# Kernel tuning notes

Hardware: AMD Instinct MI355X
Metric: run time of the kernel (lower is better)

## Reference

```python
import jax, jax.numpy as jnp
import numpy as np
import math
from jax import lax

D = 256      # d_model = out_channel
NH = 8       # n_heads
DEP = D // NH
DFF = 1024
B = 48       # conv batch == attended axis in this model
CIN = 32
HW = 32
S = 30 * 30  # (HW-2)**2 after 3x3 valid conv
OUT = 1
FMAX = float(np.finfo(np.float32).max)


def _p(k, shp, scale=0.02):
    return jax.random.normal(k, shp, jnp.float32) * scale


def setup_inputs():
    key = jax.random.key(0)
    ks = jax.random.split(key, 34)
    return {
        'X_en': jax.random.normal(ks[0], (B, CIN, HW, HW), jnp.float32),
        'X_de': jax.random.normal(ks[1], (B, CIN, HW, HW), jnp.float32),
        'conv1_w': _p(ks[2], (D, CIN, 3, 3)), 'conv1_b': _p(ks[3], (D,)),
        'conv2_w': _p(ks[4], (D, D, 3, 3)), 'conv2_b': _p(ks[5], (D,)),
        'enc_wq': _p(ks[6], (D, D)), 'enc_wk': _p(ks[7], (D, D)), 'enc_wv': _p(ks[8], (D, D)),
        'enc_rel_w': _p(ks[9], (S, NH, DEP, B)),
        'enc_ffn_w1': _p(ks[10], (DFF, D)), 'enc_ffn_b1': _p(ks[11], (DFF,)),
        'enc_ffn_w2': _p(ks[12], (D, DFF)), 'enc_ffn_b2': _p(ks[13], (D,)),
        'dec_m_wq': _p(ks[14], (D, D)), 'dec_m_wk': _p(ks[15], (D, D)), 'dec_m_wv': _p(ks[16], (D, D)),
        'dec_m_rel_w': _p(ks[17], (S, NH, DEP, B)),
        'dec_m_lin1_w': _p(ks[18], (B, B)), 'dec_m_lin1_b': _p(ks[19], (B,)),
        'dec_m_lin2_w': _p(ks[20], (B, B)), 'dec_m_lin2_b': _p(ks[21], (B,)),
        'dec_c_wq': _p(ks[22], (D, D)), 'dec_c_wk': _p(ks[23], (D, D)), 'dec_c_wv': _p(ks[24], (D, D)),
        'dec_c_rel_w': _p(ks[25], (S, NH, DEP, B)),
        'dec_ffn_w1': _p(ks[26], (DFF, D)), 'dec_ffn_b1': _p(ks[27], (DFF,)),
        'dec_ffn_w2': _p(ks[28], (D, DFF)), 'dec_ffn_b2': _p(ks[29], (D,)),
        'out_w': _p(ks[30], (OUT, D)), 'out_b': _p(ks[31], (OUT,)),
    }


def _ln(x, eps=1e-5):
    m = jnp.mean(x, -1, keepdims=True)
    v = jnp.mean((x - m) ** 2, -1, keepdims=True)
    return (x - m) / jnp.sqrt(v + eps)


def _skew(q, w):
    # Music-Transformer relative-position skew: matmul + pad + reshape + slice
    emd = jnp.einsum('shbd,shdj->shbj', q, w)  # (S,NH,b,b)
    s, h, i, j = emd.shape
    l = i + j - 1
    x = jnp.concatenate([emd, jnp.zeros_like(emd)], -1).reshape(s, h, -1)
    pad = (-x.shape[-1]) % l
    x = jnp.pad(x, ((0, 0), (0, 0), (0, pad)))
    return x.reshape(s, h, -1, l)[:, :, :i, i - 1:]


def _mha(xq, xk, xv, wq, wk, wv, rel_w, lins=None):
    b, sl, d = xq.shape
    # raw view (not transpose): (b,sl,d) -> (sl,b,NH,DEP), then swap to (sl,NH,b,DEP)
    q = (xq @ wq.T).reshape(sl, b, NH, DEP).swapaxes(1, 2)
    k = (xk @ wk.T).reshape(sl, b, NH, DEP).swapaxes(1, 2)
    v = (xv @ wv.T).reshape(sl, b, NH, DEP).swapaxes(1, 2)
    scores = jnp.einsum('shid,shjd->shij', q, k) / math.sqrt(DEP)  # (sl,NH,b,b)
    if lins is not None:  # masked path: per-call linears + causal mask
        l1w, l1b, l2w, l2b = lins
        qk = scores @ l1w.T + l1b
        qk = jnp.swapaxes(qk, 2, 3) @ l2w.T + l2b
        mask = jnp.triu(jnp.full((b, b), -FMAX, jnp.float32), 1)
        bmm = qk + mask
    else:
        bmm = scores  # linear1/linear2 outputs are discarded when mask=False
    attn = jax.nn.softmax(bmm + _skew(q, rel_w), axis=0)  # softmax over dim 0 (S)
    out = jnp.einsum('shij,shjd->shid', attn, v)  # (sl,NH,b,DEP)
    return out.reshape(b, sl, NH * DEP)  # view(a_s[2], a_s[0], -1)


def reference(X_en, X_de, conv1_w, conv1_b, conv2_w, conv2_b, enc_wq, enc_wk, enc_wv, enc_rel_w, enc_ffn_w1, enc_ffn_b1, enc_ffn_w2, enc_ffn_b2, dec_m_wq, dec_m_wk, dec_m_wv, dec_m_rel_w, dec_m_lin1_w, dec_m_lin1_b, dec_m_lin2_w, dec_m_lin2_b, dec_c_wq, dec_c_wk, dec_c_wv, dec_c_rel_w, dec_ffn_w1, dec_ffn_b1, dec_ffn_w2, dec_ffn_b2, out_w, out_b):
    def conv(x, w, b_, pad):
        y = lax.conv_general_dilated(x, w, (1, 1), [(pad, pad), (pad, pad)],
                                     dimension_numbers=('NCHW', 'OIHW', 'NCHW'))
        return y + b_[None, :, None, None]

    def convs(x):
        return conv(conv(x, conv1_w, conv1_b, 0), conv2_w, conv2_b, 1)

    xpe = convs(X_en)
    xpd = convs(X_de)
    b, d, h, w = xpe.shape
    x_en = xpe.reshape(b, h * w, d)  # raw reshape as in torch source
    x_de = xpd.reshape(b, h * w, d)
    # encoder layer
    a = _mha(x_en, x_en, x_en, enc_wq, enc_wk, enc_wv, enc_rel_w)
    o1 = _ln(x_en + a)
    f = jax.nn.relu(o1 @ enc_ffn_w1.T + enc_ffn_b1) @ enc_ffn_w2.T + enc_ffn_b2
    enc_out = _ln(o1 + f)
    # decoder layer
    m = _mha(x_de, x_de, x_de, dec_m_wq, dec_m_wk, dec_m_wv, dec_m_rel_w,
             (dec_m_lin1_w, dec_m_lin1_b, dec_m_lin2_w, dec_m_lin2_b))
    h1 = _ln(x_de + m)
    c = _mha(h1, enc_out, enc_out, dec_c_wq, dec_c_wk, dec_c_wv, dec_c_rel_w)
    h2 = _ln(c + h1)
    f2 = jax.nn.relu(h2 @ dec_ffn_w1.T + dec_ffn_b1) @ dec_ffn_w2.T + dec_ffn_b2
    h3 = _ln(h2 + f2)
    y = h3 @ out_w.T + out_b
    return jax.nn.softmax(y, axis=0)
```

## Files before the change

### kernel.cpp

```cpp
#include <hip/hip_runtime.h>
#include <float.h>

typedef __bf16 bf16;
typedef __attribute__((ext_vector_type(8))) __bf16 bf16x8;
typedef __attribute__((ext_vector_type(4))) __bf16 bf16x4;
typedef __attribute__((ext_vector_type(4))) float f32x4;

__device__ __forceinline__ int imin(int a, int b) { return a < b ? a : b; }

__device__ __forceinline__ void gl2lds(const bf16* g, bf16* l) {
  __builtin_amdgcn_global_load_lds(
      (const __attribute__((address_space(1))) void*)g,
      (__attribute__((address_space(3))) void*)l, 16, 0, 0);
}

__global__ void k_zero(bf16* zp) { zp[threadIdx.x] = (bf16)0.0f; }

struct CastSegs { const float* s[13]; bf16* d[13]; int n[13]; };
__global__ void k_cast_all(CastSegs sg, int total) {
  int i = blockIdx.x * 256 + threadIdx.x;
  if (i >= total) return;
  for (int k = 0; k < 13; ++k) {
    if (i < sg.n[k]) { sg.d[k][i] = (bf16)sg.s[k][i]; return; }
    i -= sg.n[k];
  }
}

__global__ void k_prep_rel(const float* __restrict__ rel, bf16* __restrict__ RelT) {
  int idx = blockIdx.x * 256 + threadIdx.x;
  if (idx >= 7200 * 1536) return;
  int sh = idx >> 9;  sh /= 3;
  int r = idx - sh * 1536;
  int j = r >> 5, k = r & 31;
  RelT[idx] = (bf16)rel[(size_t)sh * 1536 + k * 48 + j];
}

__global__ void k_prep_lin(const float* __restrict__ l1w, const float* __restrict__ l2w,
                           bf16* __restrict__ L1p, bf16* __restrict__ L2p) {
  for (int i = threadIdx.x; i < 3456; i += 256) {
    int r = i / 72, c = i - r * 72;
    L1p[i] = (c < 48) ? (bf16)l1w[r * 48 + c] : (bf16)0.0f;
    L2p[i] = (c < 48) ? (bf16)l2w[r * 48 + c] : (bf16)0.0f;
  }
}

__global__ void k_prep_x(const float* __restrict__ X, bf16* __restrict__ XR) {
  int idx = blockIdx.x * 256 + threadIdx.x;
  if (idx >= 48 * 1024 * 32) return;
  int b = idx >> 15, r = idx & 32767, pos = r >> 5, ic = r & 31;
  XR[idx] = (bf16)X[((size_t)(b * 32 + ic) << 10) + pos];
}

__global__ void k_pack_conv(const float* __restrict__ w, bf16* __restrict__ dst,
                            int OC, int IC, int total) {
  int idx = blockIdx.x * 256 + threadIdx.x;
  if (idx >= total) return;
  int t = idx / (OC * IC);
  int rem = idx - t * OC * IC;
  int oc = rem / IC, ic = rem - oc * IC;
  dst[idx] = (bf16)w[(size_t)(oc * IC + ic) * 9 + t];
}

__global__ __launch_bounds__(256, 2) void k_gemm128(
    const bf16* __restrict__ A, const bf16* __restrict__ B,
    const float* __restrict__ bias, bf16* __restrict__ C,
    int M, int N, int K, int relu, int ldc, int coff) {
  __shared__ alignas(16) bf16 SM[8192];
  bf16* As = SM;
  bf16* Bs = SM + 4096;
  const int t = threadIdx.x, wave = t >> 6;
  const int lane = t & 63, fr = lane & 15, kq = lane >> 4;
  const int wm = wave & 1, wn = wave >> 1;
  const int m0 = blockIdx.x * 128, n0 = blockIdx.y * 128;
  const int srow = t >> 2, kseg = (t & 3) * 8;
  f32x4 acc[4][4] = {};
  const bf16* gA0 = A + (size_t)imin(m0 + srow, M - 1) * K + kseg;
  const bf16* gA1 = A + (size_t)imin(m0 + 64 + srow, M - 1) * K + kseg;
  const bf16* gB0 = B + (size_t)(n0 + srow) * K + kseg;
  const bf16* gB1 = B + (size_t)(n0 + 64 + srow) * K + kseg;
  bf16* sA0 = As + wave * 512;
  bf16* sA1 = As + 2048 + wave * 512;
  bf16* sB0 = Bs + wave * 512;
  bf16* sB1 = Bs + 2048 + wave * 512;
  for (int k0 = 0; k0 < K; k0 += 32) {
    gl2lds(gA0 + k0, sA0);
    gl2lds(gA1 + k0, sA1);
    gl2lds(gB0 + k0, sB0);
    gl2lds(gB1 + k0, sB1);
    __syncthreads();
    bf16x8 af[4], bw[4];
    for (int mt = 0; mt < 4; ++mt)
      af[mt] = *(const bf16x8*)(As + (wm * 64 + mt * 16 + fr) * 32 + kq * 8);
    for (int nt = 0; nt < 4; ++nt)
      bw[nt] = *(const bf16x8*)(Bs + (wn * 64 + nt * 16 + fr) * 32 + kq * 8);
    for (int mt = 0; mt < 4; ++mt)
      for (int nt = 0; nt < 4; ++nt)
        acc[mt][nt] = __builtin_amdgcn_mfma_f32_16x16x32_bf16(af[mt], bw[nt], acc[mt][nt], 0, 0, 0);
    __syncthreads();
  }
  bf16* Cst = SM;
  for (int half = 0; half < 2; ++half) {
    if (wm == half) {
      for (int mt = 0; mt < 4; ++mt)
        for (int nt = 0; nt < 4; ++nt) {
          int n = n0 + wn * 64 + nt * 16 + fr;
          float bv = bias ? bias[n] : 0.0f;
          for (int r = 0; r < 4; ++r) {
            float v = acc[mt][nt][r] + bv;
            if (relu) v = fmaxf(v, 0.0f);
            Cst[(mt * 16 + kq * 4 + r) * 128 + wn * 64 + nt * 16 + fr] = (bf16)v;
          }
        }
    }
    __syncthreads();
    for (int i = t; i < 1024; i += 256) {
      int r = i >> 4, cs = i & 15;
      int gm = m0 + half * 64 + r;
      if (gm < M)
        *(bf16x8*)(C + (size_t)gm * ldc + coff + n0 + cs * 8) = *(const bf16x8*)(Cst + r * 128 + cs * 8);
    }
    __syncthreads();
  }
}

template <int CIN, int PAD, int SRCW, int SRCROWS, int CHECK, int TRANS>
__global__ __launch_bounds__(256, 2) void k_conv128(
    const bf16* __restrict__ A, const bf16* __restrict__ Bp,
    const float* __restrict__ bias, bf16* __restrict__ C,
    const bf16* __restrict__ zpage) {
  __shared__ alignas(16) bf16 SM[8192];
  bf16* As = SM;
  bf16* Bs = SM + 4096;
  const int t = threadIdx.x, wave = t >> 6;
  const int lane = t & 63, fr = lane & 15, kq = lane >> 4;
  const int wm = wave & 1, wn = wave >> 1;
  const int m0 = blockIdx.x * 128, n0 = blockIdx.y * 128;
  const int srow = t >> 2, kseg = (t & 3) * 8;
  f32x4 acc[4][4] = {};
  int bb[2], yy[2], xx[2];
  for (int hf = 0; hf < 2; ++hf) {
    int m = imin(m0 + hf * 64 + srow, 43199);
    int b = m / 900, p = m - b * 900;
    bb[hf] = b; yy[hf] = p / 30; xx[hf] = p - (p / 30) * 30;
  }
  bf16* sA0 = As + wave * 512;
  bf16* sA1 = As + 2048 + wave * 512;
  bf16* sB0 = Bs + wave * 512;
  bf16* sB1 = Bs + 2048 + wave * 512;
  for (int t9 = 0; t9 < 9; ++t9) {
    const int ky = t9 / 3, kx = t9 - ky * 3;
    const bf16* ga[2];
    for (int hf = 0; hf < 2; ++hf) {
      int sy = yy[hf] + ky - PAD, sx = xx[hf] + kx - PAD;
      bool valid = !CHECK || (sy >= 0 && sy < SRCW && sx >= 0 && sx < SRCW);
      ga[hf] = (valid ? A + (size_t)(bb[hf] * SRCROWS + sy * SRCW + sx) * CIN : zpage) + kseg;
    }
    const bf16* gb = Bp + (size_t)(t9 * 256 + n0 + srow) * CIN + kseg;
    for (int k0 = 0; k0 < CIN; k0 += 32) {
      gl2lds(ga[0] + k0, sA0);
      gl2lds(ga[1] + k0, sA1);
      gl2lds(gb + k0, sB0);
      gl2lds(gb + (size_t)64 * CIN + k0, sB1);
      __syncthreads();
      bf16x8 af[4], bw[4];
      for (int mt = 0; mt < 4; ++mt)
        af[mt] = *(const bf16x8*)(As + (wm * 64 + mt * 16 + fr) * 32 + kq * 8);
      for (int nt = 0; nt < 4; ++nt)
        bw[nt] = *(const bf16x8*)(Bs + (wn * 64 + nt * 16 + fr) * 32 + kq * 8);
      for (int mt = 0; mt < 4; ++mt)
        for (int nt = 0; nt < 4; ++nt)
          acc[mt][nt] = __builtin_amdgcn_mfma_f32_16x16x32_bf16(af[mt], bw[nt], acc[mt][nt], 0, 0, 0);
      __syncthreads();
    }
  }
  bf16* Cst = SM;
  for (int half = 0; half < 2; ++half) {
    if (wm == half) {
      for (int mt = 0; mt < 4; ++mt)
        for (int nt = 0; nt < 4; ++nt) {
          int n = n0 + wn * 64 + nt * 16 + fr;
          float bv = bias[n];
          for (int r = 0; r < 4; ++r) {
            float v = acc[mt][nt][r] + bv;
            if (TRANS)
              Cst[(wn * 64 + nt * 16 + fr) * 64 + mt * 16 + kq * 4 + r] = (bf16)v;
            else
              Cst[(mt * 16 + kq * 4 + r) * 128 + wn * 64 + nt * 16 + fr] = (bf16)v;
          }
        }
    }
    __syncthreads();
    if (TRANS) {
      for (int i = t; i < 2048; i += 256) {
        int oc = i >> 4, pc = i & 15;
        int gm = m0 + half * 64 + pc * 4;
        if (gm < 43200) {
          int b = gm / 900, p = gm - b * 900;
          *(bf16x4*)(C + (size_t)(b * 256 + n0 + oc) * 900 + p) = *(const bf16x4*)(Cst + oc * 64 + pc * 4);
        }
      }
    } else {
      for (int i = t; i < 1024; i += 256) {
        int r = i >> 4, cs = i & 15;
        int gm = m0 + half * 64 + r;
        if (gm < 43200)
          *(bf16x8*)(C + (size_t)gm * 256 + n0 + cs * 8) = *(const bf16x8*)(Cst + r * 128 + cs * 8);
      }
    }
    __syncthreads();
  }
}

template <int MASKED>
__global__ __launch_bounds__(256, MASKED ? 4 : 5) void k_attn_z(
    const bf16* __restrict__ QKV, const bf16* __restrict__ RelT, bf16* __restrict__ Z,
    const bf16* __restrict__ L1p, const bf16* __restrict__ L2p,
    const float* __restrict__ l1b, const float* __restrict__ l2b) {
  __shared__ alignas(16) bf16 QKs[2][48 * 40];
  __shared__ float EMD[48 * 49];
  __shared__ alignas(16) bf16 zst[48 * 48];
  __shared__ alignas(16) bf16 Sc[MASKED ? 48 * 72 : 8];
  __shared__ alignas(16) bf16 T2b[MASKED ? 48 * 72 : 8];
  const int sh = blockIdx.x, s = sh >> 3, h = sh & 7;
  const int t = threadIdx.x, wave = t >> 6, lane = t & 63, fr = lane & 15, kq = lane >> 4;
  const float scale = 0.17677669529663687f;
  for (int c = t; c < 384; c += 256) {
    int half = c >= 192 ? 1 : 0, cc = c - half * 192;
    int row = cc >> 2, seg = cc & 3;
    *(bf16x8*)(&QKs[half][row * 40 + seg * 8]) =
        *(const bf16x8*)(QKV + (size_t)(s * 48 + row) * 768 + half * 256 + h * 32 + seg * 8);
  }
  if constexpr (MASKED) {
    for (int i = t; i < 768; i += 256) {
      int r = i >> 4, c = 48 + (i & 15);
      Sc[r * 72 + c] = (bf16)0.0f;
      T2b[r * 72 + c] = (bf16)0.0f;
    }
  }
  __syncthreads();
  const bf16* relb = RelT + (size_t)sh * 1536;
  f32x4 sreg[3];
  int u = 0;
  for (int t9 = wave; t9 < 9; t9 += 4, ++u) {
    int ti = t9 / 3, tj = t9 - ti * 3;
    bf16x8 af = *(const bf16x8*)(&QKs[0][(ti * 16 + fr) * 40 + kq * 8]);
    bf16x8 bk = *(const bf16x8*)(&QKs[1][(tj * 16 + fr) * 40 + kq * 8]);
    bf16x8 rf = *(const bf16x8*)(relb + (tj * 16 + fr) * 32 + kq * 8);
    f32x4 sacc = {}, eacc = {};
    sacc = __builtin_amdgcn_mfma_f32_16x16x32_bf16(af, bk, sacc, 0, 0, 0);
    eacc = __builtin_amdgcn_mfma_f32_16x16x32_bf16(af, rf, eacc, 0, 0, 0);
    for (int r = 0; r < 4; ++r)
      EMD[(ti * 16 + kq * 4 + r) * 49 + tj * 16 + fr] = eacc[r];
    if constexpr (MASKED) {
      for (int r = 0; r < 4; ++r)
        Sc[(ti * 16 + kq * 4 + r) * 72 + tj * 16 + fr] = (bf16)(sacc[r] * scale);
    } else {
      for (int r = 0; r < 4; ++r) sreg[u][r] = sacc[r] * scale;
    }
  }
  __syncthreads();
  if constexpr (!MASKED) {
    u = 0;
    for (int t9 = wave; t9 < 9; t9 += 4, ++u) {
      int ti = t9 / 3, tj = t9 - ti * 3;
      for (int r = 0; r < 4; ++r) {
        int i = ti * 16 + kq * 4 + r, j = tj * 16 + fr;
        float v = sreg[u][r];
        if (j <= i) v += EMD[i * 49 + 47 + j - i];
        zst[i * 48 + j] = (bf16)v;
      }
    }
  } else {
    for (int t9 = wave; t9 < 9; t9 += 4) {
      int ti = t9 / 3, tj = t9 - ti * 3;
      f32x4 a2 = {};
      for (int k0 = 0; k0 < 64; k0 += 32) {
        bf16x8 af = *(const bf16x8*)(Sc + (ti * 16 + fr) * 72 + k0 + kq * 8);
        bf16x8 bw = *(const bf16x8*)(L1p + (tj * 16 + fr) * 72 + k0 + kq * 8);
        a2 = __builtin_amdgcn_mfma_f32_16x16x32_bf16(af, bw, a2, 0, 0, 0);
      }
      for (int r = 0; r < 4; ++r) {
        int i = ti * 16 + kq * 4 + r, a = tj * 16 + fr;
        T2b[a * 72 + i] = (bf16)(a2[r] + l1b[a]);
      }
    }
    __syncthreads();
    for (int t9 = wave; t9 < 9; t9 += 4) {
      int ti = t9 / 3, tj = t9 - ti * 3;
      f32x4 a2 = {};
      for (int k0 = 0; k0 < 64; k0 += 32) {
        bf16x8 af = *(const bf16x8*)(T2b + (ti * 16 + fr) * 72 + k0 + kq * 8);
        bf16x8 bw = *(const bf16x8*)(L2p + (tj * 16 + fr) * 72 + k0 + kq * 8);
        a2 = __builtin_amdgcn_mfma_f32_16x16x32_bf16(af, bw, a2, 0, 0, 0);
      }
      for (int r = 0; r < 4; ++r) {
        int aa = ti * 16 + kq * 4 + r, cc = tj * 16 + fr;
        float v;
        if (cc > aa) v = -10000.0f;
        else v = a2[r] + l2b[cc] + EMD[aa * 49 + 47 + cc - aa];
        zst[aa * 48 + cc] = (bf16)v;
      }
    }
  }
  __syncthreads();
  bf16* zb = Z + (size_t)sh * 2304;
  for (int c = t; c < 288; c += 256)
    *(bf16x8*)(zb + c * 8) = *(const bf16x8*)(zst + c * 8);
}

__global__ __launch_bounds__(256) void k_colstats(const bf16* __restrict__ Z,
                                                  float* __restrict__ Mc, float* __restrict__ Ic) {
  __shared__ float rm[16][17], rs[16][17];
  const int t = threadIdx.x, tc = t & 15, sg = t >> 4;
  const int col = blockIdx.x * 16 + tc;
  const bf16* p = Z + col;
  const int s0 = sg * 57, s1 = imin(900, s0 + 57);
  float m = -FLT_MAX, ssum = 0.0f;
  for (int s = s0; s < s1; ++s) {
    float v = (float)p[(size_t)s * 18432];
    if (v > m) { ssum *= __expf(m - v); m = v; }
    ssum += __expf(v - m);
  }
  rm[sg][tc] = m; rs[sg][tc] = ssum;
  __syncthreads();
  if (t < 16) {
    float M2 = -FLT_MAX;
    for (int g = 0; g < 16; ++g) M2 = fmaxf(M2, rm[g][t]);
    float S2 = 0.0f;
    for (int g = 0; g < 16; ++g) S2 += rs[g][t] * __expf(rm[g][t] - M2);
    Mc[blockIdx.x * 16 + t] = M2;
    Ic[blockIdx.x * 16 + t] = 1.0f / S2;
  }
}

__global__ __launch_bounds__(256, 6) void k_attn_av(
    const bf16* __restrict__ Z, const bf16* __restrict__ QKV,
    const float* __restrict__ Mc, const float* __restrict__ Ic, bf16* __restrict__ O) {
  __shared__ alignas(16) bf16 Ps[48 * 72];
  __shared__ alignas(16) bf16 Vt[32 * 72];
  __shared__ alignas(16) bf16 Ost[48 * 32];
  const int sh = blockIdx.x, s = sh >> 3, h = sh & 7;
  const int t = threadIdx.x, wave = t >> 6, lane = t & 63, fr = lane & 15, kq = lane >> 4;
  for (int i = t; i < 768; i += 256) Ps[(i >> 4) * 72 + 48 + (i & 15)] = (bf16)0.0f;
  for (int i = t; i < 512; i += 256) Vt[(i >> 4) * 72 + 48 + (i & 15)] = (bf16)0.0f;
  const bf16* zb = Z + (size_t)sh * 2304;
  const float* mc = Mc + h * 2304;
  const float* ic = Ic + h * 2304;
  for (int c = t; c < 288; c += 256) {
    int r = c / 6, seg = c - r * 6;
    int idx = r * 48 + seg * 8;
    bf16x8 zv = *(const bf16x8*)(zb + idx);
    f32x4 m0v = *(const f32x4*)(mc + idx), m1v = *(const f32x4*)(mc + idx + 4);
    f32x4 i0v = *(const f32x4*)(ic + idx), i1v = *(const f32x4*)(ic + idx + 4);
    bf16x8 pv;
    for (int e = 0; e < 4; ++e) pv[e] = (bf16)(__expf((float)zv[e] - m0v[e]) * i0v[e]);
    for (int e = 0; e < 4; ++e) pv[4 + e] = (bf16)(__expf((float)zv[4 + e] - m1v[e]) * i1v[e]);
    *(bf16x8*)(Ps + r * 72 + seg * 8) = pv;
  }
  for (int c = t; c < 192; c += 256) {
    int j = c >> 2, seg = c & 3;
    bf16x8 v = *(const bf16x8*)(QKV + (size_t)(s * 48 + j) * 768 + 512 + h * 32 + seg * 8);
    for (int e = 0; e < 8; ++e) Vt[(seg * 8 + e) * 72 + j] = v[e];
  }
  __syncthreads();
  for (int t6 = wave; t6 < 6; t6 += 4) {
    int ti = t6 >> 1, td = t6 & 1;
    f32x4 a2 = {};
    for (int k0 = 0; k0 < 64; k0 += 32) {
      bf16x8 af = *(const bf16x8*)(Ps + (ti * 16 + fr) * 72 + k0 + kq * 8);
      bf16x8 bv = *(const bf16x8*)(Vt + (td * 16 + fr) * 72 + k0 + kq * 8);
      a2 = __builtin_amdgcn_mfma_f32_16x16x32_bf16(af, bv, a2, 0, 0, 0);
    }
    for (int r = 0; r < 4; ++r)
      Ost[(ti * 16 + kq * 4 + r) * 32 + td * 16 + fr] = (bf16)a2[r];
  }
  __syncthreads();
  bf16* ob = O + (size_t)sh * 1536;
  for (int c = t; c < 192; c += 256)
    *(bf16x8*)(ob + c * 8) = *(const bf16x8*)(Ost + c * 8);
}

__global__ __launch_bounds__(256) void k_add_ln(
    const bf16* __restrict__ Xa, const bf16* __restrict__ Xb, bf16* __restrict__ out) {
  const int t = threadIdx.x, lane = t & 63, w = t >> 6;
  const size_t off = ((size_t)blockIdx.x * 4 + w) * 256 + lane * 4;
  bf16x4 av = *(const bf16x4*)(Xa + off);
  bf16x4 bv = *(const bf16x4*)(Xb + off);
  f32x4 x;
  for (int c = 0; c < 4; ++c) x[c] = (float)av[c] + (float)bv[c];
  float sum = x[0] + x[1] + x[2] + x[3];
  for (int o = 1; o < 64; o <<= 1) sum += __shfl_xor(sum, o);
  float mean = sum * (1.0f / 256.0f);
  float q = 0.0f;
  for (int c = 0; c < 4; ++c) { float d = x[c] - mean; q += d * d; }
  for (int o = 1; o < 64; o <<= 1) q += __shfl_xor(q, o);
  float rstd = rsqrtf(q * (1.0f / 256.0f) + 1e-5f);
  bf16x4 y;
  for (int c = 0; c < 4; ++c) y[c] = (bf16)((x[c] - mean) * rstd);
  *(bf16x4*)(out + off) = y;
}

__global__ __launch_bounds__(256) void k_ydot(
    const bf16* __restrict__ H, const float* __restrict__ w,
    const float* __restrict__ b, float* __restrict__ Y) {
  const int t = threadIdx.x, lane = t & 63, wv = t >> 6;
  const size_t row = (size_t)blockIdx.x * 4 + wv;
  bf16x4 hx = *(const bf16x4*)(H + row * 256 + lane * 4);
  f32x4 ww = *(const f32x4*)(w + lane * 4);
  float s = (float)hx[0] * ww[0] + (float)hx[1] * ww[1] + (float)hx[2] * ww[2] + (float)hx[3] * ww[3];
  for (int o = 1; o < 64; o <<= 1) s += __shfl_xor(s, o);
  if (lane == 0) Y[row] = s + b[0];
}

__global__ void k_softmax48(const float* __restrict__ Y, float* __restrict__ O) {
  int ss = blockIdx.x * 256 + threadIdx.x;
  if (ss >= 900) return;
  float m = -FLT_MAX;
  for (int b = 0; b < 48; ++b) m = fmaxf(m, Y[b * 900 + ss]);
  float sum = 0.0f;
  for (int b = 0; b < 48; ++b) sum += __expf(Y[b * 900 + ss] - m);
  float inv = 1.0f / sum;
  for (int b = 0; b < 48; ++b) O[b * 900 + ss] = __expf(Y[b * 900 + ss] - m) * inv;
}

extern "C" void kernel_launch(void* const* d_in, const int* in_sizes, int n_in,
                              void* d_out, int out_size, void* d_ws, size_t ws_size,
                              hipStream_t stream) {
  (void)in_sizes; (void)n_in; (void)out_size;
  const float* X_en = (const float*)d_in[0];
  const float* X_de = (const float*)d_in[1];
  const float* conv1_w = (const float*)d_in[2];
  const float* conv1_b = (const float*)d_in[3];
  const float* conv2_w = (const float*)d_in[4];
  const float* conv2_b = (const float*)d_in[5];
  const float* enc_wq = (const float*)d_in[6];
  const float* enc_wk = (const float*)d_in[7];
  const float* enc_wv = (const float*)d_in[8];
  const float* enc_rel = (const float*)d_in[9];
  const float* enc_f1w = (const float*)d_in[10];
  const float* enc_f1b = (const float*)d_in[11];
  const float* enc_f2w = (const float*)d_in[12];
  const float* enc_f2b = (const float*)d_in[13];
  const float* dm_wq = (const float*)d_in[14];
  const float* dm_wk = (const float*)d_in[15];
  const float* dm_wv = (const float*)d_in[16];
  const float* dm_rel = (const float*)d_in[17];
  const float* dm_l1w = (const float*)d_in[18];
  const float* dm_l1b = (const float*)d_in[19];
  const float* dm_l2w = (const float*)d_in[20];
  const float* dm_l2b = (const float*)d_in[21];
  const float* dc_wq = (const float*)d_in[22];
  const float* dc_wk = (const float*)d_in[23];
  const float* dc_wv = (const float*)d_in[24];
  const float* dc_rel = (const float*)d_in[25];
  const float* d_f1w = (const float*)d_in[26];
  const float* d_f1b = (const float*)d_in[27];
  const float* d_f2w = (const float*)d_in[28];
  const float* d_f2b = (const float*)d_in[29];
  const float* out_w = (const float*)d_in[30];
  const float* out_b = (const float*)d_in[31];
  float* OUT = (float*)d_out;

  const size_t SLOT = 22118400;
  char* ws = (char*)d_ws;
  size_t o = 0;
  bf16* S1 = (bf16*)(ws + o); o += SLOT;
  bf16* S2 = (bf16*)(ws + o); o += SLOT;
  bf16* S3 = (bf16*)(ws + o); o += SLOT;
  bf16* S4 = (bf16*)(ws + o); o += SLOT;
  bf16* S5 = (bf16*)(ws + o); o += SLOT;
  char* U = ws + o; o += 33177600 + 3 * SLOT;
  bf16* Zb = (bf16*)U;
  bf16* QKV = (bf16*)(U + 33177600);
  bf16* XR = (bf16*)U;
  bf16* C1R = (bf16*)(U + 3145728);
  bf16* HID = (bf16*)U;
  bf16* wa = (bf16*)(ws + o); o += 4603904 + 16384;
  float* Y = (float*)(ws + o); o += 172800;
  if (ws_size < o) return;

  bf16* zpage = (bf16*)Y;
  float* encM = (float*)S4; float* encI = encM + 18432;
  float* dmM  = (float*)S3; float* dmI  = dmM + 18432;
  float* crM  = (float*)S2; float* crI  = crM + 18432;
  bf16* encRel = S3;
  bf16* dmRel  = S5;
  bf16* crRel  = S3;

  bf16* c1p = wa;
  bf16* c2p = wa + 73728;
  bf16* EQKVw = wa + 663552;
  bf16* MQKVw = wa + 860160;
  bf16* cqw = wa + 1056768;
  bf16* CKVw = wa + 1122304;
  bf16* ef1 = wa + 1253376;
  bf16* ef2 = wa + 1515520;
  bf16* df1 = wa + 1777664;
  bf16* df2 = wa + 2039808;
  bf16* L1p = wa + 2301952;
  bf16* L2p = wa + 2305408;

  auto gemm = [&](const bf16* A, const bf16* B, const float* bias, bf16* C,
                  int M, int N, int K, int relu, int ldc, int coff) {
    k_gemm128<<<dim3((M + 127) / 128, N / 128), dim3(256), 0, stream>>>(
        A, B, bias, C, M, N, K, relu, ldc, coff);
  };

  k_zero<<<dim3(1), dim3(256), 0, stream>>>(zpage);
  k_pack_conv<<<dim3(288), dim3(256), 0, stream>>>(conv1_w, c1p, 256, 32, 73728);
  k_pack_conv<<<dim3(2304), dim3(256), 0, stream>>>(conv2_w, c2p, 256, 256, 589824);
  k_prep_lin<<<dim3(1), dim3(256), 0, stream>>>(dm_l1w, dm_l2w, L1p, L2p);
  {
    CastSegs sg;
    const float* srcs[13] = {enc_wq, enc_wk, enc_wv, dm_wq, dm_wk, dm_wv, dc_wq,
                             dc_wk, dc_wv, enc_f1w, enc_f2w, d_f1w, d_f2w};
    bf16* dsts[13] = {EQKVw, EQKVw + 65536, EQKVw + 131072, MQKVw, MQKVw + 65536,
                      MQKVw + 131072, cqw, CKVw, CKVw + 65536, ef1, ef2, df1, df2};
    int ns[13] = {65536, 65536, 65536, 65536, 65536, 65536, 65536, 65536, 65536,
                  262144, 262144, 262144, 262144};
    int total = 0;
    for (int k = 0; k < 13; ++k) { sg.s[k] = srcs[k]; sg.d[k] = dsts[k]; sg.n[k] = ns[k]; total += ns[k]; }
    k_cast_all<<<dim3((total + 255) / 256), dim3(256), 0, stream>>>(sg, total);
  }

  auto conv_chain = [&](const float* X, bf16* outB) {
    k_prep_x<<<dim3(6144), dim3(256), 0, stream>>>(X, XR);
    k_conv128<32, 0, 32, 1024, 0, 0><<<dim3(338, 2), dim3(256), 0, stream>>>(XR, c1p, conv1_b, C1R, zpage);
    k_conv128<256, 1, 30, 900, 1, 1><<<dim3(338, 2), dim3(256), 0, stream>>>(C1R, c2p, conv2_b, outB, zpage);
  };
  conv_chain(X_en, S1);
  conv_chain(X_de, S2);

  gemm(S1, EQKVw, nullptr, QKV, 43200, 768, 256, 0, 768, 0);
  k_prep_rel<<<dim3(43200), dim3(256), 0, stream>>>(enc_rel, encRel);
  k_attn_z<0><<<dim3(7200), dim3(256), 0, stream>>>(QKV, encRel, Zb, nullptr, nullptr, nullptr, nullptr);
  k_colstats<<<dim3(1152), dim3(256), 0, stream>>>(Zb, encM, encI);
  k_attn_av<<<dim3(7200), dim3(256), 0, stream>>>(Zb, QKV, encM, encI, S5);
  k_add_ln<<<dim3(10800), dim3(256), 0, stream>>>(S1, S5, S3);
  gemm(S3, ef1, enc_f1b, HID, 43200, 1024, 256, 1, 1024, 0);
  gemm(HID, ef2, enc_f2b, S5, 43200, 256, 1024, 0, 256, 0);
  k_add_ln<<<dim3(10800), dim3(256), 0, stream>>>(S3, S5, S1);

  gemm(S2, MQKVw, nullptr, QKV, 43200, 768, 256, 0, 768, 0);
  k_prep_rel<<<dim3(43200), dim3(256), 0, stream>>>(dm_rel, dmRel);
  k_attn_z<1><<<dim3(7200), dim3(256), 0, stream>>>(QKV, dmRel, Zb, L1p, L2p, dm_l1b, dm_l2b);
  k_colstats<<<dim3(1152), dim3(256), 0, stream>>>(Zb, dmM, dmI);
  k_attn_av<<<dim3(7200), dim3(256), 0, stream>>>(Zb, QKV, dmM, dmI, S5);
  k_add_ln<<<dim3(10800), dim3(256), 0, stream>>>(S2, S5, S4);

  gemm(S4, cqw, nullptr, QKV, 43200, 256, 256, 0, 768, 0);
  gemm(S1, CKVw, nullptr, QKV, 43200, 512, 256, 0, 768, 256);
  k_prep_rel<<<dim3(43200), dim3(256), 0, stream>>>(dc_rel, crRel);
  k_attn_z<0><<<dim3(7200), dim3(256), 0, stream>>>(QKV, crRel, Zb, nullptr, nullptr, nullptr, nullptr);
  k_colstats<<<dim3(1152), dim3(256), 0, stream>>>(Zb, crM, crI);
  k_attn_av<<<dim3(7200), dim3(256), 0, stream>>>(Zb, QKV, crM, crI, S5);
  k_add_ln<<<dim3(10800), dim3(256), 0, stream>>>(S5, S4, S3);

  gemm(S3, df1, d_f1b, HID, 43200, 1024, 256, 1, 1024, 0);
  gemm(HID, df2, d_f2b, S5, 43200, 256, 1024, 0, 256, 0);
  k_add_ln<<<dim3(10800), dim3(256), 0, stream>>>(S3, S5, S4);
  k_ydot<<<dim3(10800), dim3(256), 0, stream>>>(S4, out_w, out_b, Y);
  k_softmax48<<<dim3(4), dim3(256), 0, stream>>>(Y, OUT);
}
```

Measured before the change: 1.125 ms.

## Transpose rel weights via LDS, vectorize colstats, reorder conv loops

k_prep_rel now stages each 32x48 relative-weight slice in shared memory, so both the reads and the writes are coalesced instead of strided. Each block handles eight slices, cutting the grid from 43200 to 900 blocks. k_colstats loads eight bf16 columns per thread with one 16-byte load, shrinking its grid from 1152 to 144 blocks, which lowers parallelism for this strided reduction. The conv kernel's k-chunk and 3x3-tap loops are swapped, which only reorders the same accumulation.

```diff
diff --git a/kernel.cpp b/kernel.cpp
--- a/kernel.cpp
+++ b/kernel.cpp
@@ -26,13 +26,25 @@
   }
 }
 
-__global__ void k_prep_rel(const float* __restrict__ rel, bf16* __restrict__ RelT) {
-  int idx = blockIdx.x * 256 + threadIdx.x;
-  if (idx >= 7200 * 1536) return;
-  int sh = idx >> 9;  sh /= 3;
-  int r = idx - sh * 1536;
-  int j = r >> 5, k = r & 31;
-  RelT[idx] = (bf16)rel[(size_t)sh * 1536 + k * 48 + j];
+__global__ __launch_bounds__(256) void k_prep_rel(const float* __restrict__ rel,
+                                                  bf16* __restrict__ RelT) {
+  __shared__ float tile[32 * 49];
+  const int t = threadIdx.x;
+  for (int u = 0; u < 8; ++u) {
+    const size_t sh = (size_t)blockIdx.x * 8 + u;
+    const float* src = rel + sh * 1536;
+    bf16* dst = RelT + sh * 1536;
+    __syncthreads();
+    for (int i = t; i < 1536; i += 256) {
+      int k = i / 48, j = i - k * 48;
+      tile[k * 49 + j] = src[i];
+    }
+    __syncthreads();
+    for (int i = t; i < 1536; i += 256) {
+      int j = i >> 5, k = i & 31;
+      dst[i] = (bf16)tile[k * 49 + j];
+    }
+  }
 }
 
 __global__ void k_prep_lin(const float* __restrict__ l1w, const float* __restrict__ l2w,
@@ -147,16 +159,16 @@
   bf16* sA1 = As + 2048 + wave * 512;
   bf16* sB0 = Bs + wave * 512;
   bf16* sB1 = Bs + 2048 + wave * 512;
-  for (int t9 = 0; t9 < 9; ++t9) {
-    const int ky = t9 / 3, kx = t9 - ky * 3;
-    const bf16* ga[2];
-    for (int hf = 0; hf < 2; ++hf) {
-      int sy = yy[hf] + ky - PAD, sx = xx[hf] + kx - PAD;
-      bool valid = !CHECK || (sy >= 0 && sy < SRCW && sx >= 0 && sx < SRCW);
-      ga[hf] = (valid ? A + (size_t)(bb[hf] * SRCROWS + sy * SRCW + sx) * CIN : zpage) + kseg;
-    }
-    const bf16* gb = Bp + (size_t)(t9 * 256 + n0 + srow) * CIN + kseg;
-    for (int k0 = 0; k0 < CIN; k0 += 32) {
+  for (int k0 = 0; k0 < CIN; k0 += 32) {
+    for (int t9 = 0; t9 < 9; ++t9) {
+      const int ky = t9 / 3, kx = t9 - ky * 3;
+      const bf16* ga[2];
+      for (int hf = 0; hf < 2; ++hf) {
+        int sy = yy[hf] + ky - PAD, sx = xx[hf] + kx - PAD;
+        bool valid = !CHECK || (sy >= 0 && sy < SRCW && sx >= 0 && sx < SRCW);
+        ga[hf] = (valid ? A + (size_t)(bb[hf] * SRCROWS + sy * SRCW + sx) * CIN : zpage) + kseg;
+      }
+      const bf16* gb = Bp + (size_t)(t9 * 256 + n0 + srow) * CIN + kseg;
       gl2lds(ga[0] + k0, sA0);
       gl2lds(ga[1] + k0, sA1);
       gl2lds(gb + k0, sB0);
@@ -310,26 +322,29 @@
 
 __global__ __launch_bounds__(256) void k_colstats(const bf16* __restrict__ Z,
                                                   float* __restrict__ Mc, float* __restrict__ Ic) {
-  __shared__ float rm[16][17], rs[16][17];
-  const int t = threadIdx.x, tc = t & 15, sg = t >> 4;
-  const int col = blockIdx.x * 16 + tc;
-  const bf16* p = Z + col;
+  __shared__ float rm[16][136], rs[16][136];
+  const int t = threadIdx.x, cg = t & 15, sg = t >> 4;
+  const bf16* p = Z + blockIdx.x * 128 + cg * 8;
   const int s0 = sg * 57, s1 = imin(900, s0 + 57);
-  float m = -FLT_MAX, ssum = 0.0f;
+  float m[8], ss[8];
+  for (int e = 0; e < 8; ++e) { m[e] = -FLT_MAX; ss[e] = 0.0f; }
   for (int s = s0; s < s1; ++s) {
-    float v = (float)p[(size_t)s * 18432];
-    if (v > m) { ssum *= __expf(m - v); m = v; }
-    ssum += __expf(v - m);
-  }
-  rm[sg][tc] = m; rs[sg][tc] = ssum;
+    bf16x8 zv = *(const bf16x8*)(p + (size_t)s * 18432);
+    for (int e = 0; e < 8; ++e) {
+      float v = (float)zv[e];
+      if (v > m[e]) { ss[e] *= __expf(m[e] - v); m[e] = v; }
+      ss[e] += __expf(v - m[e]);
+    }
+  }
+  for (int e = 0; e < 8; ++e) { rm[sg][cg * 8 + e] = m[e]; rs[sg][cg * 8 + e] = ss[e]; }
   __syncthreads();
-  if (t < 16) {
+  if (t < 128) {
     float M2 = -FLT_MAX;
     for (int g = 0; g < 16; ++g) M2 = fmaxf(M2, rm[g][t]);
     float S2 = 0.0f;
     for (int g = 0; g < 16; ++g) S2 += rs[g][t] * __expf(rm[g][t] - M2);
-    Mc[blockIdx.x * 16 + t] = M2;
-    Ic[blockIdx.x * 16 + t] = 1.0f / S2;
+    Mc[blockIdx.x * 128 + t] = M2;
+    Ic[blockIdx.x * 128 + t] = 1.0f / S2;
   }
 }
 
@@ -532,9 +547,9 @@
   conv_chain(X_de, S2);
 
   gemm(S1, EQKVw, nullptr, QKV, 43200, 768, 256, 0, 768, 0);
-  k_prep_rel<<<dim3(43200), dim3(256), 0, stream>>>(enc_rel, encRel);
+  k_prep_rel<<<dim3(900), dim3(256), 0, stream>>>(enc_rel, encRel);
   k_attn_z<0><<<dim3(7200), dim3(256), 0, stream>>>(QKV, encRel, Zb, nullptr, nullptr, nullptr, nullptr);
-  k_colstats<<<dim3(1152), dim3(256), 0, stream>>>(Zb, encM, encI);
+  k_colstats<<<dim3(144), dim3(256), 0, stream>>>(Zb, encM, encI);
   k_attn_av<<<dim3(7200), dim3(256), 0, stream>>>(Zb, QKV, encM, encI, S5);
   k_add_ln<<<dim3(10800), dim3(256), 0, stream>>>(S1, S5, S3);
   gemm(S3, ef1, enc_f1b, HID, 43200, 1024, 256, 1, 1024, 0);
@@ -542,17 +557,17 @@
   k_add_ln<<<dim3(10800), dim3(256), 0, stream>>>(S3, S5, S1);
 
   gemm(S2, MQKVw, nullptr, QKV, 43200, 768, 256, 0, 768, 0);
-  k_prep_rel<<<dim3(43200), dim3(256), 0, stream>>>(dm_rel, dmRel);
+  k_prep_rel<<<dim3(900), dim3(256), 0, stream>>>(dm_rel, dmRel);
   k_attn_z<1><<<dim3(7200), dim3(256), 0, stream>>>(QKV, dmRel, Zb, L1p, L2p, dm_l1b, dm_l2b);
-  k_colstats<<<dim3(1152), dim3(256), 0, stream>>>(Zb, dmM, dmI);
+  k_colstats<<<dim3(144), dim3(256), 0, stream>>>(Zb, dmM, dmI);
   k_attn_av<<<dim3(7200), dim3(256), 0, stream>>>(Zb, QKV, dmM, dmI, S5);
   k_add_ln<<<dim3(10800), dim3(256), 0, stream>>>(S2, S5, S4);
 
   gemm(S4, cqw, nullptr, QKV, 43200, 256, 256, 0, 768, 0);
   gemm(S1, CKVw, nullptr, QKV, 43200, 512, 256, 0, 768, 256);
-  k_prep_rel<<<dim3(43200), dim3(256), 0, stream>>>(dc_rel, crRel);
+  k_prep_rel<<<dim3(900), dim3(256), 0, stream>>>(dc_rel, crRel);
   k_attn_z<0><<<dim3(7200), dim3(256), 0, stream>>>(QKV, crRel, Zb, nullptr, nullptr, nullptr, nullptr);
-  k_colstats<<<dim3(1152), dim3(256), 0, stream>>>(Zb, crM, crI);
+  k_colstats<<<dim3(144), dim3(256), 0, stream>>>(Zb, crM, crI);
   k_attn_av<<<dim3(7200), dim3(256), 0, stream>>>(Zb, QKV, crM, crI, S5);
   k_add_ln<<<dim3(10800), dim3(256), 0, stream>>>(S5, S4, S3);
 
```

Measured after the change: 1.105 ms. About the same (-1.8%).
